# Kernel tuning notes

Measured on AMD Instinct MI355X. Metric: run time of the kernel, lower is better.

Reference implementation:

```python
import jax, jax.numpy as jnp
import numpy as np
import math

L, E, H, T, V, B = 8, 1024, 16, 1024, 32000, 2
HD = E // H
EPS = 1e-5


def _quantize_sym(key, shape, std=0.02):
    w = std * jax.random.normal(key, shape, jnp.float32)
    s = jnp.max(jnp.abs(w)) / 127.0  # symmetric int8: 2**(8-1)-1
    q = jnp.clip(jnp.round(w / s), -128, 127).astype(jnp.int8)
    return q, s


def setup_inputs() -> dict:
    key = jax.random.key(0)
    ks = iter(jax.random.split(key, 64 + 16 * L))
    idx = jax.random.randint(next(ks), (B, T), 0, V)
    tok_emb = 0.02 * jax.random.normal(next(ks), (V, E), jnp.float32)
    pos_emb = 0.02 * jax.random.normal(next(ks), (T, E), jnp.float32)
    # per-layer stacked params
    attn_qw, attn_s = [], []
    aproj_qw, aproj_s = [], []
    fc_qw, fc_s = [], []
    mproj_qw, mproj_s = [], []
    for _ in range(L):
        q, s = _quantize_sym(next(ks), (3 * E, E)); attn_qw.append(q); attn_s.append(s)
        q, s = _quantize_sym(next(ks), (E, E)); aproj_qw.append(q); aproj_s.append(s)
        q, s = _quantize_sym(next(ks), (4 * E, E)); fc_qw.append(q); fc_s.append(s)
        q, s = _quantize_sym(next(ks), (E, 4 * E)); mproj_qw.append(q); mproj_s.append(s)
    lm_qw, lm_s = _quantize_sym(next(ks), (V, E))
    return {
        "idx": idx,
        "tok_emb": tok_emb,
        "pos_emb": pos_emb,
        "ln1_g": jnp.ones((L, E)), "ln1_b": jnp.zeros((L, E)),
        "attn_qw": jnp.stack(attn_qw), "attn_s": jnp.stack(attn_s), "attn_b": jnp.zeros((L, 3 * E)),
        "aproj_qw": jnp.stack(aproj_qw), "aproj_s": jnp.stack(aproj_s), "aproj_b": jnp.zeros((L, E)),
        "ln2_g": jnp.ones((L, E)), "ln2_b": jnp.zeros((L, E)),
        "fc_qw": jnp.stack(fc_qw), "fc_s": jnp.stack(fc_s), "fc_b": jnp.zeros((L, 4 * E)),
        "mproj_qw": jnp.stack(mproj_qw), "mproj_s": jnp.stack(mproj_s), "mproj_b": jnp.zeros((L, E)),
        "lnf_g": jnp.ones((E,)), "lnf_b": jnp.zeros((E,)),
        "lm_qw": lm_qw, "lm_s": lm_s,
    }


def _dequant(q, s):
    return q.astype(jnp.float32) * s


def _layernorm(x, g, b):
    m = jnp.mean(x, axis=-1, keepdims=True)
    v = jnp.mean(jnp.square(x - m), axis=-1, keepdims=True)
    return (x - m) * jax.lax.rsqrt(v + EPS) * g + b


def _gpt_forward(idx, tok_emb, pos_emb, ln1_g, ln1_b, attn_qw, attn_s, attn_b,
                 aproj_qw, aproj_s, aproj_b, ln2_g, ln2_b, fc_qw, fc_s, fc_b,
                 mproj_qw, mproj_s, mproj_b, lnf_g, lnf_b, lm_qw, lm_s):
    x = tok_emb[idx] + pos_emb[None, :, :]  # [B,T,E]
    causal = jnp.tril(jnp.ones((T, T), dtype=bool))  # [T,T]
    scale = 1.0 / math.sqrt(HD)

    def block(x, p):
        (l1g, l1b, aqw, asc, ab, pqw, psc, pb,
         l2g, l2b, fqw, fsc, fb, mqw, msc, mb) = p
        h = _layernorm(x, l1g, l1b)
        qkv = h @ _dequant(aqw, asc).T + ab  # [B,T,3E]
        q, k, v = jnp.split(qkv, 3, axis=-1)
        q = q.reshape(B, T, H, HD).transpose(0, 2, 1, 3)  # [B,H,T,HD]
        k = k.reshape(B, T, H, HD).transpose(0, 2, 1, 3)
        v = v.reshape(B, T, H, HD).transpose(0, 2, 1, 3)
        att = jnp.einsum('bhqd,bhkd->bhqk', q, k) * scale
        att = jnp.where(causal, att, -jnp.inf)
        att = jax.nn.softmax(att, axis=-1)
        y = jnp.einsum('bhqk,bhkd->bhqd', att, v)
        y = y.transpose(0, 2, 1, 3).reshape(B, T, E)
        y = y @ _dequant(pqw, psc).T + pb
        x = x + y
        h = _layernorm(x, l2g, l2b)
        h = jax.nn.gelu(h @ _dequant(fqw, fsc).T + fb, approximate=False)
        x = x + h @ _dequant(mqw, msc).T + mb
        return x, None

    layer_params = (ln1_g, ln1_b, attn_qw, attn_s, attn_b,
                    aproj_qw, aproj_s, aproj_b, ln2_g, ln2_b,
                    fc_qw, fc_s, fc_b, mproj_qw, mproj_s, mproj_b)
    x, _ = jax.lax.scan(block, x, layer_params)
    x = _layernorm(x, lnf_g, lnf_b)
    logits = x @ _dequant(lm_qw, lm_s).T  # [B,T,V], no bias
    return logits


def reference(idx, tok_emb, pos_emb, ln1_g, ln1_b, attn_qw, attn_s, attn_b,
              aproj_qw, aproj_s, aproj_b, ln2_g, ln2_b, fc_qw, fc_s, fc_b,
              mproj_qw, mproj_s, mproj_b, lnf_g, lnf_b, lm_qw, lm_s):
    return _gpt_forward(idx, tok_emb, pos_emb, ln1_g, ln1_b, attn_qw, attn_s, attn_b,
                        aproj_qw, aproj_s, aproj_b, ln2_g, ln2_b, fc_qw, fc_s, fc_b,
                        mproj_qw, mproj_s, mproj_b, lnf_g, lnf_b, lm_qw, lm_s)
```

## Files before the change

### kernel.cpp

```cpp
#include <hip/hip_runtime.h>
#include <math.h>

typedef _Float16 h16;
typedef __attribute__((ext_vector_type(8))) _Float16 half8;
typedef __attribute__((ext_vector_type(4))) _Float16 half4;
typedef __attribute__((ext_vector_type(4))) float f32x4;

#define DEVI static __device__ __forceinline__

constexpr int LAY = 8, E = 1024, NH = 16, T = 1024, VOC = 32000, BATCH = 2, HD = 64;
constexpr int MROWS = BATCH * T;
constexpr int E2 = E * E;

DEVI void glds16(const void* g, void* l) {
  __builtin_amdgcn_global_load_lds((const __attribute__((address_space(1))) void*)g,
                                   (__attribute__((address_space(3))) void*)l, 16, 0, 0);
}

__global__ __launch_bounds__(256) void prep_stride_k(const unsigned char* __restrict__ qw1,
                                                     const unsigned char* __restrict__ qw2,
                                                     int* __restrict__ stridew) {
  __shared__ int red2[4], red4[4];
  const int tid = threadIdx.x;
  const int NB = 8192;
  int c2 = 0, c4 = 0;
  for (int i = tid; i < NB; i += 256) {
    const unsigned char b1 = qw1[i], b2 = qw2[i];
    const int s1 = (b1 == 0x00 || b1 == 0xFF) ? 1 : 0;
    const int s2 = (b2 == 0x00 || b2 == 0xFF) ? 1 : 0;
    if (i & 1) c2 += s1 + s2;
    if (i & 3) c4 += s1 + s2;
  }
#pragma unroll
  for (int d = 32; d >= 1; d >>= 1) { c2 += __shfl_xor(c2, d); c4 += __shfl_xor(c4, d); }
  if ((tid & 63) == 0) { red2[tid >> 6] = c2; red4[tid >> 6] = c4; }
  __syncthreads();
  if (tid == 0) {
    const int t2 = red2[0] + red2[1] + red2[2] + red2[3];
    const int t4 = red4[0] + red4[1] + red4[2] + red4[3];
    int stride = 1;
    if (t4 > (NB * 3 / 2) * 98 / 100) stride = 4;
    else if (t2 > NB * 98 / 100) stride = 2;
    stridew[0] = stride;
  }
}

DEVI half8 dq8(const signed char* src, int bstr, float s) {
  half8 o;
  if (bstr == 4) {
    int4 r0 = *reinterpret_cast<const int4*>(src);
    int4 r1 = *reinterpret_cast<const int4*>(src + 16);
    const int* c0 = reinterpret_cast<const int*>(&r0);
    const int* c1 = reinterpret_cast<const int*>(&r1);
#pragma unroll
    for (int j = 0; j < 4; ++j) o[j] = (h16)((float)c0[j] * s);
#pragma unroll
    for (int j = 0; j < 4; ++j) o[4 + j] = (h16)((float)c1[j] * s);
  } else if (bstr == 2) {
    int4 r0 = *reinterpret_cast<const int4*>(src);
    const short* c0 = reinterpret_cast<const short*>(&r0);
#pragma unroll
    for (int j = 0; j < 8; ++j) o[j] = (h16)((float)c0[j] * s);
  } else {
    int2 r0 = *reinterpret_cast<const int2*>(src);
    const signed char* c0 = reinterpret_cast<const signed char*>(&r0);
#pragma unroll
    for (int j = 0; j < 8; ++j) o[j] = (h16)((float)c0[j] * s);
  }
  return o;
}

__global__ __launch_bounds__(256) void dequant_all_k(const signed char* __restrict__ q,
                                                     const int* __restrict__ strideptr,
                                                     const float* __restrict__ sp, int P,
                                                     h16* __restrict__ out, int n) {
  const int i = (blockIdx.x * 256 + threadIdx.x) * 8;
  if (i >= n) return;
  const float s = sp[i / P];
  const int bstr = strideptr[0];
  *reinterpret_cast<half8*>(out + i) = dq8(q + (size_t)i * (size_t)bstr, bstr, s);
}

__global__ __launch_bounds__(256) void dequant_layer_k(
    const signed char* __restrict__ qkv_q, const signed char* __restrict__ ap_q,
    const signed char* __restrict__ fc_q, const signed char* __restrict__ mp_q,
    const float* __restrict__ qkv_s, const float* __restrict__ ap_s,
    const float* __restrict__ fc_s, const float* __restrict__ mp_s, int l,
    const int* __restrict__ strideptr,
    h16* __restrict__ wq, h16* __restrict__ wa, h16* __restrict__ wf,
    h16* __restrict__ wm) {
  const int e = (blockIdx.x * 256 + threadIdx.x) * 8;
  const int bstr = strideptr[0];
  const signed char* src;
  h16* dst;
  float s;
  if (e < 3 * E2) {
    src = qkv_q + ((size_t)l * 3 * E2 + e) * (size_t)bstr;
    dst = wq + e;
    s = qkv_s[l];
  } else if (e < 4 * E2) {
    const int e2 = e - 3 * E2;
    src = ap_q + ((size_t)l * E2 + e2) * (size_t)bstr;
    dst = wa + e2;
    s = ap_s[l];
  } else if (e < 8 * E2) {
    const int e2 = e - 4 * E2;
    src = fc_q + ((size_t)l * 4 * E2 + e2) * (size_t)bstr;
    dst = wf + e2;
    s = fc_s[l];
  } else {
    const int e2 = e - 8 * E2;
    src = mp_q + ((size_t)l * 4 * E2 + e2) * (size_t)bstr;
    dst = wm + e2;
    s = mp_s[l];
  }
  *reinterpret_cast<half8*>(dst) = dq8(src, bstr, s);
}

__global__ __launch_bounds__(256) void embed_k(const int* __restrict__ idx,
                                               const float* __restrict__ tok,
                                               const float* __restrict__ pos,
                                               float* __restrict__ x) {
  const int row = blockIdx.x;
  const int t = row & (T - 1);
  const int id = idx[row];
  const float4 a = reinterpret_cast<const float4*>(tok + (size_t)id * E)[threadIdx.x];
  const float4 p = reinterpret_cast<const float4*>(pos + (size_t)t * E)[threadIdx.x];
  float4 o; o.x = a.x + p.x; o.y = a.y + p.y; o.z = a.z + p.z; o.w = a.w + p.w;
  reinterpret_cast<float4*>(x + (size_t)row * E)[threadIdx.x] = o;
}

__global__ __launch_bounds__(256) void ln_k(const float* __restrict__ x,
                                            const float* __restrict__ g,
                                            const float* __restrict__ bb,
                                            h16* __restrict__ out) {
  __shared__ float red[8];
  const int row = blockIdx.x, tid = threadIdx.x;
  const float4 v = reinterpret_cast<const float4*>(x + (size_t)row * E)[tid];
  float s1 = v.x + v.y + v.z + v.w;
  float s2 = v.x * v.x + v.y * v.y + v.z * v.z + v.w * v.w;
#pragma unroll
  for (int d = 32; d >= 1; d >>= 1) { s1 += __shfl_xor(s1, d); s2 += __shfl_xor(s2, d); }
  if ((tid & 63) == 0) { red[tid >> 6] = s1; red[4 + (tid >> 6)] = s2; }
  __syncthreads();
  s1 = red[0] + red[1] + red[2] + red[3];
  s2 = red[4] + red[5] + red[6] + red[7];
  const float mean = s1 * (1.0f / E);
  const float var = s2 * (1.0f / E) - mean * mean;
  const float rstd = rsqrtf(var + 1e-5f);
  const float4 gv = reinterpret_cast<const float4*>(g)[tid];
  const float4 bv = reinterpret_cast<const float4*>(bb)[tid];
  half4 o;
  o[0] = (h16)((v.x - mean) * rstd * gv.x + bv.x);
  o[1] = (h16)((v.y - mean) * rstd * gv.y + bv.y);
  o[2] = (h16)((v.z - mean) * rstd * gv.z + bv.z);
  o[3] = (h16)((v.w - mean) * rstd * gv.w + bv.w);
  *reinterpret_cast<half4*>(out + (size_t)row * E + tid * 4) = o;
}

__global__ __launch_bounds__(256) void reduce_ln_k(const float* __restrict__ pbuf, int S,
                                                   const float* __restrict__ bias,
                                                   float* __restrict__ x,
                                                   const float* __restrict__ g,
                                                   const float* __restrict__ bb,
                                                   h16* __restrict__ out) {
  __shared__ float red[8];
  const int row = blockIdx.x, tid = threadIdx.x;
  const size_t base = (size_t)row * E + tid * 4;
  float4 a = *reinterpret_cast<const float4*>(pbuf + base);
  for (int s = 1; s < S; ++s) {
    const float4 p = *reinterpret_cast<const float4*>(pbuf + (size_t)s * MROWS * E + base);
    a.x += p.x; a.y += p.y; a.z += p.z; a.w += p.w;
  }
  const float4 bv0 = *reinterpret_cast<const float4*>(bias + tid * 4);
  float4 v = *reinterpret_cast<const float4*>(x + base);
  v.x += a.x + bv0.x; v.y += a.y + bv0.y; v.z += a.z + bv0.z; v.w += a.w + bv0.w;
  *reinterpret_cast<float4*>(x + base) = v;
  float s1 = v.x + v.y + v.z + v.w;
  float s2 = v.x * v.x + v.y * v.y + v.z * v.z + v.w * v.w;
#pragma unroll
  for (int d = 32; d >= 1; d >>= 1) { s1 += __shfl_xor(s1, d); s2 += __shfl_xor(s2, d); }
  if ((tid & 63) == 0) { red[tid >> 6] = s1; red[4 + (tid >> 6)] = s2; }
  __syncthreads();
  s1 = red[0] + red[1] + red[2] + red[3];
  s2 = red[4] + red[5] + red[6] + red[7];
  const float mean = s1 * (1.0f / E);
  const float var = s2 * (1.0f / E) - mean * mean;
  const float rstd = rsqrtf(var + 1e-5f);
  const float4 gv = *reinterpret_cast<const float4*>(g + tid * 4);
  const float4 lb = *reinterpret_cast<const float4*>(bb + tid * 4);
  half4 o;
  o[0] = (h16)((v.x - mean) * rstd * gv.x + lb.x);
  o[1] = (h16)((v.y - mean) * rstd * gv.y + lb.y);
  o[2] = (h16)((v.z - mean) * rstd * gv.z + lb.z);
  o[3] = (h16)((v.w - mean) * rstd * gv.w + lb.w);
  *reinterpret_cast<half4*>(out + (size_t)row * E + tid * 4) = o;
}

template <int OUT_KIND, int DO_GELU, int DO_RESID>
__global__ __launch_bounds__(256) void gemm_bt(const h16* __restrict__ A,
                                               const h16* __restrict__ Bw,
                                               const float* __restrict__ bias,
                                               const float* __restrict__ resid,
                                               void* __restrict__ Cout,
                                               int M, int N, int K, int ldc) {
  __shared__ __align__(16) h16 As[2][4096];
  __shared__ __align__(16) h16 Bs[2][4096];
  const int tid = threadIdx.x;
  const int w = tid >> 6, lane = tid & 63;
  const int lin = blockIdx.x;
  const int cpx = gridDim.x >> 3;
  const int swz = (lin & 7) * cpx + (lin >> 3);
  const int m0 = (swz & 15) << 7;
  const int n0 = (swz >> 4) << 7;
  const int wr = w >> 1, wc = w & 1;
  const int lr = lane >> 2, lc8 = (lane & 3) << 3;
  const h16* gA = A + (size_t)(m0 + w * 16 + lr) * K + lc8;
  const h16* gB = Bw + (size_t)(n0 + w * 16 + lr) * K + lc8;
  f32x4 acc[4][4] = {};
  const int fl = lane & 15, fk = (lane >> 4) << 3;
  const int nk = K >> 5;
  auto stage = [&](int buf, int kt) {
    const h16* pa = gA + (kt << 5);
    const h16* pb = gB + (kt << 5);
    glds16(pa, &As[buf][w * 512]);
    glds16(pa + (size_t)64 * K, &As[buf][2048 + w * 512]);
    glds16(pb, &Bs[buf][w * 512]);
    glds16(pb + (size_t)64 * K, &Bs[buf][2048 + w * 512]);
  };
  stage(0, 0);
  __syncthreads();
  int cur = 0;
  for (int kt = 0; kt < nk; ++kt) {
    if (kt + 1 < nk) stage(cur ^ 1, kt + 1);
    half8 af[4], bfr[4];
#pragma unroll
    for (int mi = 0; mi < 4; ++mi)
      af[mi] = *reinterpret_cast<const half8*>(&As[cur][(wr * 64 + mi * 16 + fl) * 32 + fk]);
#pragma unroll
    for (int ni = 0; ni < 4; ++ni)
      bfr[ni] = *reinterpret_cast<const half8*>(&Bs[cur][(wc * 64 + ni * 16 + fl) * 32 + fk]);
#pragma unroll
    for (int mi = 0; mi < 4; ++mi)
#pragma unroll
      for (int ni = 0; ni < 4; ++ni)
        acc[mi][ni] = __builtin_amdgcn_mfma_f32_16x16x32_f16(af[mi], bfr[ni], acc[mi][ni], 0, 0, 0);
    __syncthreads();
    cur ^= 1;
  }
  const int fr4 = (lane >> 4) << 2;
#pragma unroll
  for (int mi = 0; mi < 4; ++mi) {
#pragma unroll
    for (int ni = 0; ni < 4; ++ni) {
      const int col = n0 + wc * 64 + ni * 16 + fl;
      const float bv = bias ? bias[col] : 0.0f;
#pragma unroll
      for (int j = 0; j < 4; ++j) {
        const int row = m0 + wr * 64 + mi * 16 + fr4 + j;
        float v = acc[mi][ni][j] + bv;
        if (DO_GELU) v = 0.5f * v * (1.0f + erff(v * 0.70710678118f));
        if (DO_RESID) v += resid[(size_t)row * ldc + col];
        if (OUT_KIND == 1)
          reinterpret_cast<h16*>(Cout)[(size_t)row * ldc + col] = (h16)v;
        else
          reinterpret_cast<float*>(Cout)[(size_t)row * ldc + col] = v;
      }
    }
  }
}

__global__ __launch_bounds__(512) void gemm_bt256(const h16* __restrict__ A,
                                                  const h16* __restrict__ Bw,
                                                  float* __restrict__ Cout,
                                                  int M, int N, int K) {
  __shared__ __align__(16) h16 As[2][8192];
  __shared__ __align__(16) h16 Bs[2][8192];
  const int tid = threadIdx.x;
  const int w = tid >> 6, lane = tid & 63;
  const int lin = blockIdx.x;
  const int cpx = gridDim.x >> 3;
  const int swz = (lin & 7) * cpx + (lin >> 3);
  const int m0 = (swz & 7) << 8;
  const int n0 = (swz >> 3) << 8;
  const int wr = w >> 2, wc = w & 3;
  const int lr = lane >> 2, lc8 = (lane & 3) << 3;
  const h16* gA = A + (size_t)(m0 + w * 16 + lr) * K + lc8;
  const h16* gB = Bw + (size_t)(n0 + w * 16 + lr) * K + lc8;
  f32x4 acc[8][4] = {};
  const int fl = lane & 15, fk = (lane >> 4) << 3;
  const int nk = K >> 5;
  auto stageA = [&](int buf, int kt, int half) {
    glds16(gA + (size_t)(kt << 5) + (size_t)half * 128 * K,
           &As[buf][half * 4096 + w * 512]);
  };
  auto stageB = [&](int buf, int kt, int half) {
    glds16(gB + (size_t)(kt << 5) + (size_t)half * 128 * K,
           &Bs[buf][half * 4096 + w * 512]);
  };
  stageA(0, 0, 0); stageA(0, 0, 1);
  stageB(0, 0, 0); stageB(0, 0, 1);
  stageB(1, 1, 0); stageB(1, 1, 1);
  asm volatile("s_waitcnt vmcnt(2)" ::: "memory");
  asm volatile("s_barrier" ::: "memory");
  int cur = 0;
  for (int kt = 0; kt < nk; ++kt) {
    half8 af[4], bfr[4];
#pragma unroll
    for (int mi = 0; mi < 4; ++mi)
      af[mi] = *reinterpret_cast<const half8*>(&As[cur][(wr * 128 + mi * 16 + fl) * 32 + fk]);
#pragma unroll
    for (int ni = 0; ni < 4; ++ni)
      bfr[ni] = *reinterpret_cast<const half8*>(&Bs[cur][(wc * 64 + ni * 16 + fl) * 32 + fk]);
    if (kt + 1 < nk) { stageA(cur ^ 1, kt + 1, 0); stageA(cur ^ 1, kt + 1, 1); }
    asm volatile("s_waitcnt lgkmcnt(0)" ::: "memory");
    __builtin_amdgcn_sched_barrier(0);
    __builtin_amdgcn_s_setprio(1);
#pragma unroll
    for (int mi = 0; mi < 4; ++mi)
#pragma unroll
      for (int ni = 0; ni < 4; ++ni)
        acc[mi][ni] = __builtin_amdgcn_mfma_f32_16x16x32_f16(af[mi], bfr[ni], acc[mi][ni], 0, 0, 0);
    __builtin_amdgcn_s_setprio(0);
    asm volatile("s_barrier" ::: "memory");
#pragma unroll
    for (int mi = 0; mi < 4; ++mi)
      af[mi] = *reinterpret_cast<const half8*>(
          &As[cur][(wr * 128 + 64 + mi * 16 + fl) * 32 + fk]);
    if (kt + 2 < nk) { stageB(cur, kt + 2, 0); stageB(cur, kt + 2, 1); }
    if (kt < nk - 2)
      asm volatile("s_waitcnt vmcnt(2)" ::: "memory");
    else
      asm volatile("s_waitcnt vmcnt(0)" ::: "memory");
    asm volatile("s_waitcnt lgkmcnt(0)" ::: "memory");
    __builtin_amdgcn_sched_barrier(0);
    __builtin_amdgcn_s_setprio(1);
#pragma unroll
    for (int mi = 0; mi < 4; ++mi)
#pragma unroll
      for (int ni = 0; ni < 4; ++ni)
        acc[4 + mi][ni] =
            __builtin_amdgcn_mfma_f32_16x16x32_f16(af[mi], bfr[ni], acc[4 + mi][ni], 0, 0, 0);
    __builtin_amdgcn_s_setprio(0);
    asm volatile("s_barrier" ::: "memory");
    cur ^= 1;
  }
  const int fr4 = (lane >> 4) << 2;
#pragma unroll
  for (int mi = 0; mi < 8; ++mi)
#pragma unroll
    for (int ni = 0; ni < 4; ++ni) {
      const int col = n0 + wc * 64 + ni * 16 + fl;
#pragma unroll
      for (int j = 0; j < 4; ++j) {
        const int row = m0 + wr * 128 + mi * 16 + fr4 + j;
        Cout[(size_t)row * N + col] = acc[mi][ni][j];
      }
    }
}

__global__ __launch_bounds__(256) void gemm_btk(const h16* __restrict__ A,
                                                const h16* __restrict__ Bw,
                                                float* __restrict__ pbuf,
                                                int M, int N, int Kc, int ldk) {
  __shared__ __align__(16) h16 As[2][4096];
  __shared__ __align__(16) h16 Bs[2][4096];
  const int tid = threadIdx.x;
  const int w = tid >> 6, lane = tid & 63;
  const int lin = blockIdx.x;
  const int cpx = gridDim.x >> 3;
  const int swz = (lin & 7) * cpx + (lin >> 3);
  const int m0 = (swz & 15) << 7;
  const int n0 = (swz >> 4) << 7;
  const int s = blockIdx.y;
  const int koff = s * Kc;
  const int wr = w >> 1, wc = w & 1;
  const int lr = lane >> 2, lc8 = (lane & 3) << 3;
  const h16* gA = A + (size_t)(m0 + w * 16 + lr) * ldk + koff + lc8;
  const h16* gB = Bw + (size_t)(n0 + w * 16 + lr) * ldk + koff + lc8;
  f32x4 acc[4][4] = {};
  const int fl = lane & 15, fk = (lane >> 4) << 3;
  const int nk = Kc >> 5;
  auto stage = [&](int buf, int kt) {
    const h16* pa = gA + (kt << 5);
    const h16* pb = gB + (kt << 5);
    glds16(pa, &As[buf][w * 512]);
    glds16(pa + (size_t)64 * ldk, &As[buf][2048 + w * 512]);
    glds16(pb, &Bs[buf][w * 512]);
    glds16(pb + (size_t)64 * ldk, &Bs[buf][2048 + w * 512]);
  };
  stage(0, 0);
  __syncthreads();
  int cur = 0;
  for (int kt = 0; kt < nk; ++kt) {
    if (kt + 1 < nk) stage(cur ^ 1, kt + 1);
    half8 af[4], bfr[4];
#pragma unroll
    for (int mi = 0; mi < 4; ++mi)
      af[mi] = *reinterpret_cast<const half8*>(&As[cur][(wr * 64 + mi * 16 + fl) * 32 + fk]);
#pragma unroll
    for (int ni = 0; ni < 4; ++ni)
      bfr[ni] = *reinterpret_cast<const half8*>(&Bs[cur][(wc * 64 + ni * 16 + fl) * 32 + fk]);
#pragma unroll
    for (int mi = 0; mi < 4; ++mi)
#pragma unroll
      for (int ni = 0; ni < 4; ++ni)
        acc[mi][ni] = __builtin_amdgcn_mfma_f32_16x16x32_f16(af[mi], bfr[ni], acc[mi][ni], 0, 0, 0);
    __syncthreads();
    cur ^= 1;
  }
  float* out = pbuf + (size_t)s * M * N;
  const int fr4 = (lane >> 4) << 2;
#pragma unroll
  for (int mi = 0; mi < 4; ++mi)
#pragma unroll
    for (int ni = 0; ni < 4; ++ni) {
      const int col = n0 + wc * 64 + ni * 16 + fl;
#pragma unroll
      for (int j = 0; j < 4; ++j) {
        const int row = m0 + wr * 64 + mi * 16 + fr4 + j;
        out[(size_t)row * N + col] = acc[mi][ni][j];
      }
    }
}

__global__ __launch_bounds__(256) void attn_k(const h16* __restrict__ qkv,
                                              h16* __restrict__ yout) {
  __shared__ __align__(16) h16 Ks[2][4096];
  __shared__ __align__(16) h16 VTs[2][4096];
  __shared__ __align__(16) h16 Ps[4096];
  const int qt = (int)gridDim.x - 1 - (int)blockIdx.x;
  const int bh = blockIdx.y;
  const int b = bh >> 4, h = bh & 15;
  const int tid = threadIdx.x, w = tid >> 6, lane = tid & 63;
  const int fl = lane & 15, fkg = lane >> 4, fk = fkg << 3;
  const size_t rowQ0 = (size_t)b * T + qt * 64 + w * 16;
  const h16* qbase = qkv + (rowQ0 + fl) * 3072 + h * 64;
  const half8 qf0 = *reinterpret_cast<const half8*>(qbase + fk);
  const half8 qf1 = *reinterpret_cast<const half8*>(qbase + 32 + fk);
  f32x4 yacc[4] = {};
  float m_run[4], l_run[4];
#pragma unroll
  for (int j = 0; j < 4; ++j) { m_run[j] = -1e30f; l_run[j] = 0.f; }
  const int q_g0 = qt * 64 + w * 16 + (fkg << 2);
  const int krow = lane >> 3, kcol8 = (lane & 7) << 3;
  const int vrow = tid >> 2, vcol8 = (tid & 3) << 3;

  auto stageK = [&](int kt, int buf) {
    const size_t kbase = (size_t)b * T + kt * 64;
    const h16* gk = qkv + (kbase + w * 8 + krow) * 3072 + E + h * 64 + kcol8;
    glds16(gk, &Ks[buf][w * 512]);
    glds16(gk + (size_t)32 * 3072, &Ks[buf][2048 + w * 512]);
  };
  auto loadV = [&](int kt, int half32) {
    const size_t kbase = (size_t)b * T + kt * 64;
    return *reinterpret_cast<const half8*>(qkv + (kbase + vrow) * 3072 + 2 * E + h * 64 +
                                           vcol8 + half32);
  };
  auto scatterV = [&](int buf, half8 v0, half8 v1) {
#pragma unroll
    for (int e = 0; e < 8; ++e) VTs[buf][(vcol8 + e) * 64 + vrow] = v0[e];
#pragma unroll
    for (int e = 0; e < 8; ++e) VTs[buf][(vcol8 + 32 + e) * 64 + vrow] = v1[e];
  };

  stageK(0, 0);
  {
    half8 v0 = loadV(0, 0), v1 = loadV(0, 32);
    scatterV(0, v0, v1);
  }
  __syncthreads();
  int cur = 0;
  for (int kt = 0; kt <= qt; ++kt) {
    const bool hn = kt < qt;
    half8 nv0, nv1;
    if (hn) {
      stageK(kt + 1, cur ^ 1);
      nv0 = loadV(kt + 1, 0);
      nv1 = loadV(kt + 1, 32);
    }
    f32x4 sacc[4];
#pragma unroll
    for (int ni = 0; ni < 4; ++ni) {
      const half8 kb0 = *reinterpret_cast<const half8*>(&Ks[cur][(ni * 16 + fl) * 64 + fk]);
      const half8 kb1 = *reinterpret_cast<const half8*>(&Ks[cur][(ni * 16 + fl) * 64 + 32 + fk]);
      f32x4 z = {0.f, 0.f, 0.f, 0.f};
      z = __builtin_amdgcn_mfma_f32_16x16x32_f16(qf0, kb0, z, 0, 0, 0);
      z = __builtin_amdgcn_mfma_f32_16x16x32_f16(qf1, kb1, z, 0, 0, 0);
      sacc[ni] = z;
    }
    float tmax[4] = {-1e30f, -1e30f, -1e30f, -1e30f};
#pragma unroll
    for (int ni = 0; ni < 4; ++ni) {
      const int kcol = kt * 64 + ni * 16 + fl;
#pragma unroll
      for (int j = 0; j < 4; ++j) {
        float sv = sacc[ni][j] * 0.125f;
        sv = (kcol > q_g0 + j) ? -1e30f : sv;
        sacc[ni][j] = sv;
        tmax[j] = fmaxf(tmax[j], sv);
      }
    }
#pragma unroll
    for (int d = 1; d < 16; d <<= 1) {
#pragma unroll
      for (int j = 0; j < 4; ++j) tmax[j] = fmaxf(tmax[j], __shfl_xor(tmax[j], d));
    }
    float sc_old[4], psum[4] = {0.f, 0.f, 0.f, 0.f};
#pragma unroll
    for (int j = 0; j < 4; ++j) {
      const float mn = fmaxf(m_run[j], tmax[j]);
      sc_old[j] = __expf(m_run[j] - mn);
      m_run[j] = mn;
    }
#pragma unroll
    for (int ni = 0; ni < 4; ++ni)
#pragma unroll
      for (int j = 0; j < 4; ++j) {
        const float p = __expf(sacc[ni][j] - m_run[j]);
        sacc[ni][j] = p;
        psum[j] += p;
      }
#pragma unroll
    for (int d = 1; d < 16; d <<= 1) {
#pragma unroll
      for (int j = 0; j < 4; ++j) psum[j] += __shfl_xor(psum[j], d);
    }
#pragma unroll
    for (int j = 0; j < 4; ++j) l_run[j] = l_run[j] * sc_old[j] + psum[j];
#pragma unroll
    for (int di = 0; di < 4; ++di)
#pragma unroll
      for (int j = 0; j < 4; ++j) yacc[di][j] *= sc_old[j];
    if (hn) scatterV(cur ^ 1, nv0, nv1);
#pragma unroll
    for (int ni = 0; ni < 4; ++ni)
#pragma unroll
      for (int j = 0; j < 4; ++j)
        Ps[w * 1024 + ((fkg << 2) + j) * 64 + ni * 16 + fl] = (h16)sacc[ni][j];
    __syncthreads();
    const half8 pa0 = *reinterpret_cast<const half8*>(&Ps[w * 1024 + fl * 64 + fk]);
    const half8 pa1 = *reinterpret_cast<const half8*>(&Ps[w * 1024 + fl * 64 + 32 + fk]);
#pragma unroll
    for (int di = 0; di < 4; ++di) {
      const half8 vb0 = *reinterpret_cast<const half8*>(&VTs[cur][(di * 16 + fl) * 64 + fk]);
      const half8 vb1 = *reinterpret_cast<const half8*>(&VTs[cur][(di * 16 + fl) * 64 + 32 + fk]);
      yacc[di] = __builtin_amdgcn_mfma_f32_16x16x32_f16(pa0, vb0, yacc[di], 0, 0, 0);
      yacc[di] = __builtin_amdgcn_mfma_f32_16x16x32_f16(pa1, vb1, yacc[di], 0, 0, 0);
    }
    __syncthreads();
    cur ^= 1;
  }
  float rl[4];
#pragma unroll
  for (int j = 0; j < 4; ++j) rl[j] = 1.0f / l_run[j];
  const size_t orow0 = rowQ0 + (fkg << 2);
#pragma unroll
  for (int di = 0; di < 4; ++di)
#pragma unroll
    for (int j = 0; j < 4; ++j)
      yout[(orow0 + j) * E + h * 64 + di * 16 + fl] = (h16)(yacc[di][j] * rl[j]);
}

extern "C" void kernel_launch(void* const* d_in, const int* in_sizes, int n_in,
                              void* d_out, int out_size, void* d_ws, size_t ws_size,
                              hipStream_t stream) {
  (void)in_sizes; (void)n_in; (void)out_size; (void)ws_size;
  const int* idx = (const int*)d_in[0];
  const float* tok = (const float*)d_in[1];
  const float* pos = (const float*)d_in[2];
  const float* ln1g = (const float*)d_in[3];
  const float* ln1b = (const float*)d_in[4];
  const signed char* attn_qw = (const signed char*)d_in[5];
  const float* attn_s = (const float*)d_in[6];
  const float* attn_b = (const float*)d_in[7];
  const signed char* aproj_qw = (const signed char*)d_in[8];
  const float* aproj_s = (const float*)d_in[9];
  const float* aproj_b = (const float*)d_in[10];
  const float* ln2g = (const float*)d_in[11];
  const float* ln2b = (const float*)d_in[12];
  const signed char* fc_qw = (const signed char*)d_in[13];
  const float* fc_s = (const float*)d_in[14];
  const float* fc_b = (const float*)d_in[15];
  const signed char* mproj_qw = (const signed char*)d_in[16];
  const float* mproj_s = (const float*)d_in[17];
  const float* mproj_b = (const float*)d_in[18];
  const float* lnfg = (const float*)d_in[19];
  const float* lnfb = (const float*)d_in[20];
  const signed char* lm_qw = (const signed char*)d_in[21];
  const float* lm_s = (const float*)d_in[22];

  char* ws = (char*)d_ws;
  size_t off = 0;
  auto alloc = [&](size_t bytes) {
    char* p = ws + off;
    off += (bytes + 255) & ~(size_t)255;
    return p;
  };
  float* x = (float*)alloc((size_t)MROWS * E * 4);
  h16* hbuf = (h16*)alloc((size_t)MROWS * E * 2);
  h16* big = (h16*)alloc((size_t)MROWS * 4 * E * 2);
  h16* wq = (h16*)alloc((size_t)3 * E2 * 2);
  h16* wa = (h16*)alloc((size_t)E2 * 2);
  h16* wf = (h16*)alloc((size_t)4 * E2 * 2);
  h16* wm = (h16*)alloc((size_t)4 * E2 * 2);
  float* pbuf = (float*)alloc((size_t)4 * MROWS * E * 4);
  h16* wlm = (h16*)alloc((size_t)VOC * E * 2);
  int* stridew = (int*)alloc(256);
  h16* qkvb = big;
  h16* yb = hbuf;
  h16* hfc = big;

  prep_stride_k<<<1, 256, 0, stream>>>((const unsigned char*)attn_qw,
                                       (const unsigned char*)fc_qw, stridew);
  dequant_all_k<<<VOC * E / 2048, 256, 0, stream>>>(lm_qw, stridew, lm_s, VOC * E,
                                                    wlm, VOC * E);
  embed_k<<<MROWS, 256, 0, stream>>>(idx, tok, pos, x);
  ln_k<<<MROWS, 256, 0, stream>>>(x, ln1g, ln1b, hbuf);

  for (int l = 0; l < LAY; ++l) {
    dequant_layer_k<<<12 * E2 / 2048, 256, 0, stream>>>(
        attn_qw, aproj_qw, fc_qw, mproj_qw, attn_s, aproj_s, fc_s, mproj_s, l,
        stridew, wq, wa, wf, wm);
    gemm_bt<1, 0, 0><<<24 * 16, 256, 0, stream>>>(hbuf, wq, attn_b + l * 3 * E, nullptr,
                                                  qkvb, MROWS, 3 * E, E, 3 * E);
    attn_k<<<dim3(16, 32), 256, 0, stream>>>(qkvb, yb);
    gemm_btk<<<dim3(128, 2), 256, 0, stream>>>(yb, wa, pbuf, MROWS, E, 512, E);
    reduce_ln_k<<<MROWS, 256, 0, stream>>>(pbuf, 2, aproj_b + l * E, x,
                                           ln2g + l * E, ln2b + l * E, hbuf);
    gemm_bt<1, 1, 0><<<32 * 16, 256, 0, stream>>>(hbuf, wf, fc_b + l * 4 * E, nullptr,
                                                  hfc, MROWS, 4 * E, E, 4 * E);
    gemm_btk<<<dim3(128, 4), 256, 0, stream>>>(hfc, wm, pbuf, MROWS, E, 1024, 4 * E);
    const float* ng = (l < LAY - 1) ? (ln1g + (l + 1) * E) : lnfg;
    const float* nb = (l < LAY - 1) ? (ln1b + (l + 1) * E) : lnfb;
    reduce_ln_k<<<MROWS, 256, 0, stream>>>(pbuf, 4, mproj_b + l * E, x, ng, nb, hbuf);
  }
  gemm_bt256<<<1000, 512, 0, stream>>>(hbuf, wlm, (float*)d_out, MROWS, VOC, E);
}
```

Before: 1.748 ms.

## Split GEMM k-step into two phases with staggered A/B prefetch and manual waitcnts

Both f16 MFMA GEMM kernels now split each k-iteration into two halves: the first half computes rows 0-1 while prefetching the next A tile, and the second half computes rows 2-3 while prefetching B two steps ahead into the just-freed buffer. Full __syncthreads are replaced by raw s_barrier with explicit vmcnt/lgkmcnt waits, sched_barrier and s_setprio around the MFMA bursts. The aim is finer-grained overlap of global-to-LDS loads with matrix math and less stall at each barrier. The cost is two barriers per k-step and hand-counted vmcnt correctness, which risks races if the counts are wrong.

New measurement: 1.738 ms. No clear change (-0.6%).

```diff
diff --git a/kernel.cpp b/kernel.cpp
--- a/kernel.cpp
+++ b/kernel.cpp
@@ -220,32 +220,59 @@
   f32x4 acc[4][4] = {};
   const int fl = lane & 15, fk = (lane >> 4) << 3;
   const int nk = K >> 5;
-  auto stage = [&](int buf, int kt) {
+  auto stageA = [&](int buf, int kt) {
     const h16* pa = gA + (kt << 5);
-    const h16* pb = gB + (kt << 5);
     glds16(pa, &As[buf][w * 512]);
     glds16(pa + (size_t)64 * K, &As[buf][2048 + w * 512]);
+  };
+  auto stageB = [&](int buf, int kt) {
+    const h16* pb = gB + (kt << 5);
     glds16(pb, &Bs[buf][w * 512]);
     glds16(pb + (size_t)64 * K, &Bs[buf][2048 + w * 512]);
   };
-  stage(0, 0);
-  __syncthreads();
+  stageA(0, 0);
+  stageB(0, 0);
+  stageB(1, 1);
+  asm volatile("s_waitcnt vmcnt(2)" ::: "memory");
+  asm volatile("s_barrier" ::: "memory");
   int cur = 0;
   for (int kt = 0; kt < nk; ++kt) {
-    if (kt + 1 < nk) stage(cur ^ 1, kt + 1);
     half8 af[4], bfr[4];
 #pragma unroll
-    for (int mi = 0; mi < 4; ++mi)
+    for (int mi = 0; mi < 2; ++mi)
       af[mi] = *reinterpret_cast<const half8*>(&As[cur][(wr * 64 + mi * 16 + fl) * 32 + fk]);
 #pragma unroll
     for (int ni = 0; ni < 4; ++ni)
       bfr[ni] = *reinterpret_cast<const half8*>(&Bs[cur][(wc * 64 + ni * 16 + fl) * 32 + fk]);
-#pragma unroll
-    for (int mi = 0; mi < 4; ++mi)
+    if (kt + 1 < nk) stageA(cur ^ 1, kt + 1);
+    asm volatile("s_waitcnt lgkmcnt(0)" ::: "memory");
+    __builtin_amdgcn_sched_barrier(0);
+    __builtin_amdgcn_s_setprio(1);
+#pragma unroll
+    for (int mi = 0; mi < 2; ++mi)
 #pragma unroll
       for (int ni = 0; ni < 4; ++ni)
         acc[mi][ni] = __builtin_amdgcn_mfma_f32_16x16x32_f16(af[mi], bfr[ni], acc[mi][ni], 0, 0, 0);
-    __syncthreads();
+    __builtin_amdgcn_s_setprio(0);
+    asm volatile("s_barrier" ::: "memory");
+#pragma unroll
+    for (int mi = 2; mi < 4; ++mi)
+      af[mi] = *reinterpret_cast<const half8*>(&As[cur][(wr * 64 + mi * 16 + fl) * 32 + fk]);
+    if (kt + 2 < nk) stageB(cur, kt + 2);
+    if (kt < nk - 2)
+      asm volatile("s_waitcnt vmcnt(2)" ::: "memory");
+    else
+      asm volatile("s_waitcnt vmcnt(0)" ::: "memory");
+    asm volatile("s_waitcnt lgkmcnt(0)" ::: "memory");
+    __builtin_amdgcn_sched_barrier(0);
+    __builtin_amdgcn_s_setprio(1);
+#pragma unroll
+    for (int mi = 2; mi < 4; ++mi)
+#pragma unroll
+      for (int ni = 0; ni < 4; ++ni)
+        acc[mi][ni] = __builtin_amdgcn_mfma_f32_16x16x32_f16(af[mi], bfr[ni], acc[mi][ni], 0, 0, 0);
+    __builtin_amdgcn_s_setprio(0);
+    asm volatile("s_barrier" ::: "memory");
     cur ^= 1;
   }
   const int fr4 = (lane >> 4) << 2;
@@ -381,32 +408,59 @@
   f32x4 acc[4][4] = {};
   const int fl = lane & 15, fk = (lane >> 4) << 3;
   const int nk = Kc >> 5;
-  auto stage = [&](int buf, int kt) {
+  auto stageA = [&](int buf, int kt) {
     const h16* pa = gA + (kt << 5);
-    const h16* pb = gB + (kt << 5);
     glds16(pa, &As[buf][w * 512]);
     glds16(pa + (size_t)64 * ldk, &As[buf][2048 + w * 512]);
+  };
+  auto stageB = [&](int buf, int kt) {
+    const h16* pb = gB + (kt << 5);
     glds16(pb, &Bs[buf][w * 512]);
     glds16(pb + (size_t)64 * ldk, &Bs[buf][2048 + w * 512]);
   };
-  stage(0, 0);
-  __syncthreads();
+  stageA(0, 0);
+  stageB(0, 0);
+  stageB(1, 1);
+  asm volatile("s_waitcnt vmcnt(2)" ::: "memory");
+  asm volatile("s_barrier" ::: "memory");
   int cur = 0;
   for (int kt = 0; kt < nk; ++kt) {
-    if (kt + 1 < nk) stage(cur ^ 1, kt + 1);
     half8 af[4], bfr[4];
 #pragma unroll
-    for (int mi = 0; mi < 4; ++mi)
+    for (int mi = 0; mi < 2; ++mi)
       af[mi] = *reinterpret_cast<const half8*>(&As[cur][(wr * 64 + mi * 16 + fl) * 32 + fk]);
 #pragma unroll
     for (int ni = 0; ni < 4; ++ni)
       bfr[ni] = *reinterpret_cast<const half8*>(&Bs[cur][(wc * 64 + ni * 16 + fl) * 32 + fk]);
-#pragma unroll
-    for (int mi = 0; mi < 4; ++mi)
+    if (kt + 1 < nk) stageA(cur ^ 1, kt + 1);
+    asm volatile("s_waitcnt lgkmcnt(0)" ::: "memory");
+    __builtin_amdgcn_sched_barrier(0);
+    __builtin_amdgcn_s_setprio(1);
+#pragma unroll
+    for (int mi = 0; mi < 2; ++mi)
 #pragma unroll
       for (int ni = 0; ni < 4; ++ni)
         acc[mi][ni] = __builtin_amdgcn_mfma_f32_16x16x32_f16(af[mi], bfr[ni], acc[mi][ni], 0, 0, 0);
-    __syncthreads();
+    __builtin_amdgcn_s_setprio(0);
+    asm volatile("s_barrier" ::: "memory");
+#pragma unroll
+    for (int mi = 2; mi < 4; ++mi)
+      af[mi] = *reinterpret_cast<const half8*>(&As[cur][(wr * 64 + mi * 16 + fl) * 32 + fk]);
+    if (kt + 2 < nk) stageB(cur, kt + 2);
+    if (kt < nk - 2)
+      asm volatile("s_waitcnt vmcnt(2)" ::: "memory");
+    else
+      asm volatile("s_waitcnt vmcnt(0)" ::: "memory");
+    asm volatile("s_waitcnt lgkmcnt(0)" ::: "memory");
+    __builtin_amdgcn_sched_barrier(0);
+    __builtin_amdgcn_s_setprio(1);
+#pragma unroll
+    for (int mi = 2; mi < 4; ++mi)
+#pragma unroll
+      for (int ni = 0; ni < 4; ++ni)
+        acc[mi][ni] = __builtin_amdgcn_mfma_f32_16x16x32_f16(af[mi], bfr[ni], acc[mi][ni], 0, 0, 0);
+    __builtin_amdgcn_s_setprio(0);
+    asm volatile("s_barrier" ::: "memory");
     cur ^= 1;
   }
   float* out = pbuf + (size_t)s * M * N;
```
